# Performance work log

Hardware: AMD Instinct MI355X
Metric: run time of the kernel (lower is better)

## Reference

```python
import jax, jax.numpy as jnp
import numpy as np

B = 262144
P = 0.8
CLS_NUM_LIST = [500, 477, 456, 435, 415, 396, 378, 361, 345, 329, 314, 300, 286, 273, 261, 249, 238, 227, 217, 207, 197, 188, 180, 172, 164, 156, 149, 142, 136, 130, 124, 118, 113, 108, 103, 98, 94, 90, 85, 82, 78, 74, 71, 68, 65, 62, 59, 56, 54, 51, 49, 47, 45, 43, 41, 39, 37, 35, 34, 32, 31, 29, 28, 27, 26, 24, 23, 22, 21, 20, 19, 18, 18, 17, 16, 15, 15, 14, 13, 13, 12, 12, 11, 11, 10, 10, 9, 9, 8, 8, 8, 7, 7, 7, 6, 6, 6, 5, 5, 5]
C = len(CLS_NUM_LIST)


def _build_weight_matrix():
    n = np.asarray(CLS_NUM_LIST, dtype=np.float64).reshape(C, 1)
    wm = (1.0 / n) * n.T            # wm[i, j] = n_j / n_i
    wm[wm > 1] = 1.0
    wm = np.power(wm, P)
    return jnp.asarray(wm, dtype=jnp.float32)


def setup_inputs() -> dict:
    key = jax.random.key(0)
    kx, kt = jax.random.split(key)
    x = jax.random.normal(kx, (B, C), dtype=jnp.float32)
    target = jax.random.randint(kt, (B,), 0, C, dtype=jnp.int64)
    weight_matrix = _build_weight_matrix()                      # [C, C]
    neg_grad = jnp.full((1, C), 1e-06, dtype=jnp.float32)
    pos_grad = jnp.full((1, C), 1e-06, dtype=jnp.float32)
    return {"x": x, "target": target, "weight_matrix": weight_matrix,
            "neg_grad": neg_grad, "pos_grad": pos_grad}


def reference(x, target, weight_matrix, neg_grad, pos_grad):
    bs, num_classes = x.shape
    onehot = jax.nn.one_hot(target, num_classes, dtype=x.dtype)   # [B, C]
    # one_hot @ weight_matrix is algebraically a row gather
    weight = weight_matrix[target]                                # [B, C]
    weighted_x = x + jnp.log(weight)
    log_sm = jax.nn.log_softmax(weighted_x, axis=1)               # stable log(softmax)
    softmax_x = jnp.exp(log_sm)
    # grad-statistic accumulation (detached in the original)
    grad = jnp.abs(softmax_x - onehot)
    neg_grad_new = neg_grad + (grad * (1.0 - onehot)).sum(0)      # [1, C]
    pos_grad_new = pos_grad + (grad * onehot).sum(0)              # [1, C]
    ratio = pos_grad_new / neg_grad_new
    loss = -jnp.sum(onehot * log_sm) / bs
    return loss, neg_grad_new, pos_grad_new, ratio
```

## Files before the change

### kernel.cpp

```cpp
#include <hip/hip_runtime.h>

#define NCLS 100
#define NROWS 262144
#define MAIN_BLOCKS 2048
#define MAIN_THREADS 256
#define NWAVES (MAIN_THREADS / 64)
#define NOCT ((MAIN_BLOCKS * MAIN_THREADS) / 8)
#define ROWS_PER_OCT (NROWS / NOCT)
#define PART_LD MAIN_BLOCKS
#define NPART (2 * NCLS + 1)
#define WS_NEEDED ((size_t)NPART * PART_LD * 4)

#define LOADX(buf, rp) do {                                                    \
    buf[0] = (rp)[k];                                                          \
    buf[1] = (rp)[8 + k];                                                      \
    buf[2] = (rp)[16 + k];                                                     \
    buf[3] = (k == 0) ? (rp)[24] : make_float4(0.f, 0.f, 0.f, 0.f);            \
} while (0)

#define COMPROW(buf, LGT, VTX, TT) do {                                        \
    float4 e[4];                                                               \
    float sp = 0.f;                                                            \
    _Pragma("unroll")                                                          \
    for (int m = 0; m < 4; ++m) {                                              \
        if (8 * m + k < 25) {                                                  \
            e[m].x = __expf(buf[m].x + fminf(lgn[m].x - (LGT), 0.f));          \
            e[m].y = __expf(buf[m].y + fminf(lgn[m].y - (LGT), 0.f));          \
            e[m].z = __expf(buf[m].z + fminf(lgn[m].z - (LGT), 0.f));          \
            e[m].w = __expf(buf[m].w + fminf(lgn[m].w - (LGT), 0.f));          \
            sp += (e[m].x + e[m].y) + (e[m].z + e[m].w);                       \
        } else {                                                               \
            e[m] = make_float4(0.f, 0.f, 0.f, 0.f);                            \
        }                                                                      \
    }                                                                          \
    float s = sp + __shfl_xor(sp, 1, 64);                                      \
    s += __shfl_xor(s, 2, 64);                                                 \
    s += __shfl_xor(s, 4, 64);                                                 \
    const float inv_s = 1.0f / s;                                              \
    if (k == 0) {                                                              \
        loss_local += __logf(s) - (VTX);                                       \
        const float pt = __expf(VTX) * inv_s;                                  \
        atomicAdd(&lds_q[TT], pt);                                             \
        atomicAdd(&lds_pos[TT], 1.0f - pt);                                    \
    }                                                                          \
    _Pragma("unroll")                                                          \
    for (int m = 0; m < 4; ++m) {                                              \
        if (8 * m + k < 25) {                                                  \
            S4[m].x = fmaf(e[m].x, inv_s, S4[m].x);                            \
            S4[m].y = fmaf(e[m].y, inv_s, S4[m].y);                            \
            S4[m].z = fmaf(e[m].z, inv_s, S4[m].z);                            \
            S4[m].w = fmaf(e[m].w, inv_s, S4[m].w);                            \
        }                                                                      \
    }                                                                          \
} while (0)

__global__ __launch_bounds__(MAIN_THREADS, 4)
void seesaw_main(const float* __restrict__ x,
                 const int* __restrict__ target,
                 const float* __restrict__ wm,
                 float* __restrict__ part,
                 float* __restrict__ out,
                 int use_part) {
    __shared__ float lds_lgn[NCLS];
    __shared__ float lds_q[NCLS];
    __shared__ float lds_pos[NCLS];
    __shared__ float lds_S[NWAVES][NCLS];
    __shared__ float lds_loss[NWAVES];

    if (threadIdx.x < NCLS) {
        lds_lgn[threadIdx.x] = __logf(wm[threadIdx.x]);
        lds_q[threadIdx.x] = 0.f;
        lds_pos[threadIdx.x] = 0.f;
    }
    __syncthreads();

    const int lane = threadIdx.x & 63;
    const int wave = threadIdx.x >> 6;
    const int k    = threadIdx.x & 7;
    const int oct  = (blockIdx.x * MAIN_THREADS + threadIdx.x) >> 3;

    float4 lgn[4];
#pragma unroll
    for (int m = 0; m < 4; ++m) {
        const int g = 8 * m + k;
        if (g < 25) {
            lgn[m].x = lds_lgn[4 * g + 0];
            lgn[m].y = lds_lgn[4 * g + 1];
            lgn[m].z = lds_lgn[4 * g + 2];
            lgn[m].w = lds_lgn[4 * g + 3];
        } else {
            lgn[m] = make_float4(0.f, 0.f, 0.f, 0.f);
        }
    }

    int tr[ROWS_PER_OCT];
    float vtx[ROWS_PER_OCT], lgt[ROWS_PER_OCT];
    const float4* xr[ROWS_PER_OCT];
#pragma unroll
    for (int r = 0; r < ROWS_PER_OCT; ++r) {
        const int row = oct + r * NOCT;
        tr[r] = target[row];
        xr[r] = reinterpret_cast<const float4*>(x + (size_t)row * NCLS);
    }
#pragma unroll
    for (int r = 0; r < ROWS_PER_OCT; ++r) {
        vtx[r] = x[(size_t)(oct + r * NOCT) * NCLS + tr[r]];
        lgt[r] = lds_lgn[tr[r]];
    }

    float4 S4[4];
#pragma unroll
    for (int m = 0; m < 4; ++m) S4[m] = make_float4(0.f, 0.f, 0.f, 0.f);
    float loss_local = 0.0f;

    float4 xv0[4], xv1[4];
    LOADX(xv0, xr[0]);
    LOADX(xv1, xr[1]);
    COMPROW(xv0, lgt[0], vtx[0], tr[0]);
    LOADX(xv0, xr[2]);
    COMPROW(xv1, lgt[1], vtx[1], tr[1]);
    LOADX(xv1, xr[3]);
    COMPROW(xv0, lgt[2], vtx[2], tr[2]);
    COMPROW(xv1, lgt[3], vtx[3], tr[3]);

#pragma unroll
    for (int m = 0; m < 4; ++m) {
#pragma unroll
        for (int msk = 8; msk <= 32; msk <<= 1) {
            S4[m].x += __shfl_xor(S4[m].x, msk, 64);
            S4[m].y += __shfl_xor(S4[m].y, msk, 64);
            S4[m].z += __shfl_xor(S4[m].z, msk, 64);
            S4[m].w += __shfl_xor(S4[m].w, msk, 64);
        }
    }
#pragma unroll
    for (int msk = 1; msk < 64; msk <<= 1)
        loss_local += __shfl_xor(loss_local, msk, 64);
    if (lane == 0) lds_loss[wave] = loss_local;

    if (lane < 8) {
#pragma unroll
        for (int m = 0; m < 4; ++m) {
            const int g = 8 * m + lane;
            if (g < 25) {
                lds_S[wave][4 * g + 0] = S4[m].x;
                lds_S[wave][4 * g + 1] = S4[m].y;
                lds_S[wave][4 * g + 2] = S4[m].z;
                lds_S[wave][4 * g + 3] = S4[m].w;
            }
        }
    }
    __syncthreads();

    if (use_part) {
        if (threadIdx.x < NCLS) {
            const int j = threadIdx.x;
            float sb = 0.f;
#pragma unroll
            for (int w = 0; w < NWAVES; ++w) sb += lds_S[w][j];
            part[(size_t)j * PART_LD + blockIdx.x] = sb - lds_q[j];
            part[(size_t)(NCLS + j) * PART_LD + blockIdx.x] = lds_pos[j];
        }
        if (threadIdx.x == 0) {
            float l = 0.f;
#pragma unroll
            for (int w = 0; w < NWAVES; ++w) l += lds_loss[w];
            part[(size_t)(2 * NCLS) * PART_LD + blockIdx.x] = l;
        }
    } else {
        if (threadIdx.x < NCLS) {
            const int j = threadIdx.x;
            float sb = 0.f;
#pragma unroll
            for (int w = 0; w < NWAVES; ++w) sb += lds_S[w][j];
            atomicAdd(&out[1 + j], sb - lds_q[j]);
            atomicAdd(&out[1 + NCLS + j], lds_pos[j]);
        }
        if (threadIdx.x == 0) {
            float l = 0.f;
#pragma unroll
            for (int w = 0; w < NWAVES; ++w) l += lds_loss[w];
            atomicAdd(&out[0], l);
        }
    }
}

__global__ void seesaw_tail(const float* __restrict__ part,
                            const float* __restrict__ neg_in,
                            const float* __restrict__ pos_in,
                            float* __restrict__ out) {
    const int c = blockIdx.x;
    __shared__ float redn[NWAVES], redp[NWAVES];
    const int lane = threadIdx.x & 63;
    const int wave = threadIdx.x >> 6;

    float sn = 0.f, sp = 0.f;
    if (c < NCLS) {
        for (int b = threadIdx.x; b < MAIN_BLOCKS; b += MAIN_THREADS) {
            sn += part[(size_t)c * PART_LD + b];
            sp += part[(size_t)(NCLS + c) * PART_LD + b];
        }
    } else {
        for (int b = threadIdx.x; b < MAIN_BLOCKS; b += MAIN_THREADS)
            sn += part[(size_t)(2 * NCLS) * PART_LD + b];
    }
#pragma unroll
    for (int msk = 1; msk < 64; msk <<= 1) {
        sn += __shfl_xor(sn, msk, 64);
        sp += __shfl_xor(sp, msk, 64);
    }
    if (lane == 0) { redn[wave] = sn; redp[wave] = sp; }
    __syncthreads();
    if (threadIdx.x == 0) {
        float tn = 0.f, tp = 0.f;
#pragma unroll
        for (int w = 0; w < NWAVES; ++w) { tn += redn[w]; tp += redp[w]; }
        if (c < NCLS) {
            const float neg = neg_in[c] + tn;
            const float pos = pos_in[c] + tp;
            out[1 + c] = neg;
            out[1 + NCLS + c] = pos;
            out[1 + 2 * NCLS + c] = pos / neg;
        } else {
            out[0] = tn * (1.0f / (float)NROWS);
        }
    }
}

__global__ void seesaw_init(const float* __restrict__ neg_in,
                            const float* __restrict__ pos_in,
                            float* __restrict__ out) {
    int i = threadIdx.x;
    if (i == 0) out[0] = 0.0f;
    if (i < NCLS) {
        out[1 + i] = neg_in[i];
        out[1 + NCLS + i] = pos_in[i];
    }
}

__global__ void seesaw_fin(float* __restrict__ out) {
    int j = threadIdx.x;
    if (j == 0) out[0] *= (1.0f / (float)NROWS);
    if (j < NCLS) out[1 + 2 * NCLS + j] = out[1 + NCLS + j] / out[1 + j];
}

extern "C" void kernel_launch(void* const* d_in, const int* in_sizes, int n_in,
                              void* d_out, int out_size, void* d_ws, size_t ws_size,
                              hipStream_t stream) {
    const float* x      = (const float*)d_in[0];
    const int*   target = (const int*)d_in[1];
    const float* wm     = (const float*)d_in[2];
    const float* neg_in = (const float*)d_in[3];
    const float* pos_in = (const float*)d_in[4];
    float* out  = (float*)d_out;
    float* part = (float*)d_ws;
    const int use_part = (ws_size >= WS_NEEDED) ? 1 : 0;

    if (use_part) {
        hipLaunchKernelGGL(seesaw_main, dim3(MAIN_BLOCKS), dim3(MAIN_THREADS), 0, stream,
                           x, target, wm, part, out, 1);
        hipLaunchKernelGGL(seesaw_tail, dim3(NCLS + 1), dim3(MAIN_THREADS), 0, stream,
                           part, neg_in, pos_in, out);
    } else {
        hipLaunchKernelGGL(seesaw_init, dim3(1), dim3(256), 0, stream,
                           neg_in, pos_in, out);
        hipLaunchKernelGGL(seesaw_main, dim3(MAIN_BLOCKS), dim3(MAIN_THREADS), 0, stream,
                           x, target, wm, part, out, 0);
        hipLaunchKernelGGL(seesaw_fin, dim3(1), dim3(128), 0, stream, out);
    }
}
```

Before: 32.37 us.

## Fuse main pass and tail reduction into one cooperative kernel with grid sync

Adds a cooperative kernel that computes per-block partials, publishes them with agent-scope stores, performs a grid-wide sync, then has the first 101 blocks reduce the partials and write final outputs. This removes the second kernel launch and its launch gap. Launch bounds rise to 8 blocks per CU so all 2048 blocks can be co-resident; it falls back to the two-kernel path if occupancy or the cooperative launch fails. Risks include grid-sync overhead, a per-call occupancy query on the host, and register pressure from the tighter launch bound.

```diff
diff --git a/kernel.cpp b/kernel.cpp
--- a/kernel.cpp
+++ b/kernel.cpp
@@ -1,4 +1,5 @@
 #include <hip/hip_runtime.h>
+#include <hip/hip_cooperative_groups.h>
 
 #define NCLS 100
 #define NROWS 262144
@@ -8,8 +9,9 @@
 #define NOCT ((MAIN_BLOCKS * MAIN_THREADS) / 8)
 #define ROWS_PER_OCT (NROWS / NOCT)
 #define PART_LD MAIN_BLOCKS
-#define NPART (2 * NCLS + 1)
-#define WS_NEEDED ((size_t)NPART * PART_LD * 4)
+#define NPC (2 * NCLS + 1)
+#define WS_NEEDED ((size_t)NPC * PART_LD * 4)
+
 
 #define LOADX(buf, rp) do {                                                    \
     buf[0] = (rp)[k];                                                          \
@@ -54,6 +56,175 @@
     }                                                                          \
 } while (0)
 
+__device__ __forceinline__ void seesaw_body(
+    const float* __restrict__ x, const int* __restrict__ target,
+    const float* __restrict__ wm,
+    float* lds_lgn, float* lds_q, float* lds_pos,
+    float* lds_S , float* lds_loss) {
+
+    if (threadIdx.x < NCLS) {
+        lds_lgn[threadIdx.x] = __logf(wm[threadIdx.x]);
+        lds_q[threadIdx.x] = 0.f;
+        lds_pos[threadIdx.x] = 0.f;
+    }
+    __syncthreads();
+
+    const int lane = threadIdx.x & 63;
+    const int wave = threadIdx.x >> 6;
+    const int k    = threadIdx.x & 7;
+    const int oct  = (blockIdx.x * MAIN_THREADS + threadIdx.x) >> 3;
+
+    float4 lgn[4];
+#pragma unroll
+    for (int m = 0; m < 4; ++m) {
+        const int g = 8 * m + k;
+        if (g < 25) {
+            lgn[m].x = lds_lgn[4 * g + 0];
+            lgn[m].y = lds_lgn[4 * g + 1];
+            lgn[m].z = lds_lgn[4 * g + 2];
+            lgn[m].w = lds_lgn[4 * g + 3];
+        } else {
+            lgn[m] = make_float4(0.f, 0.f, 0.f, 0.f);
+        }
+    }
+
+    int tr[ROWS_PER_OCT];
+    float vtx[ROWS_PER_OCT], lgt[ROWS_PER_OCT];
+    const float4* xr[ROWS_PER_OCT];
+#pragma unroll
+    for (int r = 0; r < ROWS_PER_OCT; ++r) {
+        const int row = oct + r * NOCT;
+        tr[r] = target[row];
+        xr[r] = reinterpret_cast<const float4*>(x + (size_t)row * NCLS);
+    }
+#pragma unroll
+    for (int r = 0; r < ROWS_PER_OCT; ++r) {
+        vtx[r] = x[(size_t)(oct + r * NOCT) * NCLS + tr[r]];
+        lgt[r] = lds_lgn[tr[r]];
+    }
+
+    float4 S4[4];
+#pragma unroll
+    for (int m = 0; m < 4; ++m) S4[m] = make_float4(0.f, 0.f, 0.f, 0.f);
+    float loss_local = 0.0f;
+
+    float4 xv0[4], xv1[4];
+    LOADX(xv0, xr[0]);
+    LOADX(xv1, xr[1]);
+    COMPROW(xv0, lgt[0], vtx[0], tr[0]);
+    LOADX(xv0, xr[2]);
+    COMPROW(xv1, lgt[1], vtx[1], tr[1]);
+    LOADX(xv1, xr[3]);
+    COMPROW(xv0, lgt[2], vtx[2], tr[2]);
+    COMPROW(xv1, lgt[3], vtx[3], tr[3]);
+
+#pragma unroll
+    for (int m = 0; m < 4; ++m) {
+#pragma unroll
+        for (int msk = 8; msk <= 32; msk <<= 1) {
+            S4[m].x += __shfl_xor(S4[m].x, msk, 64);
+            S4[m].y += __shfl_xor(S4[m].y, msk, 64);
+            S4[m].z += __shfl_xor(S4[m].z, msk, 64);
+            S4[m].w += __shfl_xor(S4[m].w, msk, 64);
+        }
+    }
+#pragma unroll
+    for (int msk = 1; msk < 64; msk <<= 1)
+        loss_local += __shfl_xor(loss_local, msk, 64);
+    if (lane == 0) lds_loss[wave] = loss_local;
+
+    if (lane < 8) {
+#pragma unroll
+        for (int m = 0; m < 4; ++m) {
+            const int g = 8 * m + lane;
+            if (g < 25) {
+                lds_S[wave * NCLS + 4 * g + 0] = S4[m].x;
+                lds_S[wave * NCLS + 4 * g + 1] = S4[m].y;
+                lds_S[wave * NCLS + 4 * g + 2] = S4[m].z;
+                lds_S[wave * NCLS + 4 * g + 3] = S4[m].w;
+            }
+        }
+    }
+    __syncthreads();
+}
+
+__global__ __launch_bounds__(MAIN_THREADS, 8)
+void seesaw_coop(const float* __restrict__ x,
+                 const int* __restrict__ target,
+                 const float* __restrict__ wm,
+                 float* __restrict__ part,
+                 const float* __restrict__ neg_in,
+                 const float* __restrict__ pos_in,
+                 float* __restrict__ out) {
+    __shared__ float lds_lgn[NCLS];
+    __shared__ float lds_q[NCLS];
+    __shared__ float lds_pos[NCLS];
+    __shared__ float lds_S[NWAVES * NCLS];
+    __shared__ float lds_loss[NWAVES];
+    __shared__ float redn[NWAVES], redp[NWAVES];
+
+    seesaw_body(x, target, wm, lds_lgn, lds_q, lds_pos, lds_S, lds_loss);
+
+    if (threadIdx.x < NCLS) {
+        const int j = threadIdx.x;
+        float sb = 0.f;
+#pragma unroll
+        for (int w = 0; w < NWAVES; ++w) sb += lds_S[w * NCLS + j];
+        __hip_atomic_store(&part[(size_t)j * PART_LD + blockIdx.x], sb - lds_q[j],
+                           __ATOMIC_RELAXED, __HIP_MEMORY_SCOPE_AGENT);
+        __hip_atomic_store(&part[(size_t)(NCLS + j) * PART_LD + blockIdx.x], lds_pos[j],
+                           __ATOMIC_RELAXED, __HIP_MEMORY_SCOPE_AGENT);
+    }
+    if (threadIdx.x == 0) {
+        float l = 0.f;
+#pragma unroll
+        for (int w = 0; w < NWAVES; ++w) l += lds_loss[w];
+        __hip_atomic_store(&part[(size_t)(2 * NCLS) * PART_LD + blockIdx.x], l,
+                           __ATOMIC_RELAXED, __HIP_MEMORY_SCOPE_AGENT);
+    }
+    __threadfence();
+    cooperative_groups::this_grid().sync();
+
+    const int c = blockIdx.x;
+    if (c > NCLS) return;
+    const int lane = threadIdx.x & 63;
+    const int wave = threadIdx.x >> 6;
+    float sn = 0.f, sp2 = 0.f;
+    if (c < NCLS) {
+        for (int b = threadIdx.x; b < PART_LD; b += MAIN_THREADS) {
+            sn  += __hip_atomic_load(&part[(size_t)c * PART_LD + b],
+                                     __ATOMIC_RELAXED, __HIP_MEMORY_SCOPE_AGENT);
+            sp2 += __hip_atomic_load(&part[(size_t)(NCLS + c) * PART_LD + b],
+                                     __ATOMIC_RELAXED, __HIP_MEMORY_SCOPE_AGENT);
+        }
+    } else {
+        for (int b = threadIdx.x; b < PART_LD; b += MAIN_THREADS)
+            sn += __hip_atomic_load(&part[(size_t)(2 * NCLS) * PART_LD + b],
+                                    __ATOMIC_RELAXED, __HIP_MEMORY_SCOPE_AGENT);
+    }
+#pragma unroll
+    for (int msk = 1; msk < 64; msk <<= 1) {
+        sn += __shfl_xor(sn, msk, 64);
+        sp2 += __shfl_xor(sp2, msk, 64);
+    }
+    if (lane == 0) { redn[wave] = sn; redp[wave] = sp2; }
+    __syncthreads();
+    if (threadIdx.x == 0) {
+        float tn = 0.f, tp = 0.f;
+#pragma unroll
+        for (int w = 0; w < NWAVES; ++w) { tn += redn[w]; tp += redp[w]; }
+        if (c < NCLS) {
+            const float neg = neg_in[c] + tn;
+            const float pos = pos_in[c] + tp;
+            out[1 + c] = neg;
+            out[1 + NCLS + c] = pos;
+            out[1 + 2 * NCLS + c] = pos / neg;
+        } else {
+            out[0] = tn * (1.0f / (float)NROWS);
+        }
+    }
+}
+
 __global__ __launch_bounds__(MAIN_THREADS, 4)
 void seesaw_main(const float* __restrict__ x,
                  const int* __restrict__ target,
@@ -64,100 +235,17 @@
     __shared__ float lds_lgn[NCLS];
     __shared__ float lds_q[NCLS];
     __shared__ float lds_pos[NCLS];
-    __shared__ float lds_S[NWAVES][NCLS];
+    __shared__ float lds_S[NWAVES * NCLS];
     __shared__ float lds_loss[NWAVES];
 
-    if (threadIdx.x < NCLS) {
-        lds_lgn[threadIdx.x] = __logf(wm[threadIdx.x]);
-        lds_q[threadIdx.x] = 0.f;
-        lds_pos[threadIdx.x] = 0.f;
-    }
-    __syncthreads();
-
-    const int lane = threadIdx.x & 63;
-    const int wave = threadIdx.x >> 6;
-    const int k    = threadIdx.x & 7;
-    const int oct  = (blockIdx.x * MAIN_THREADS + threadIdx.x) >> 3;
-
-    float4 lgn[4];
-#pragma unroll
-    for (int m = 0; m < 4; ++m) {
-        const int g = 8 * m + k;
-        if (g < 25) {
-            lgn[m].x = lds_lgn[4 * g + 0];
-            lgn[m].y = lds_lgn[4 * g + 1];
-            lgn[m].z = lds_lgn[4 * g + 2];
-            lgn[m].w = lds_lgn[4 * g + 3];
-        } else {
-            lgn[m] = make_float4(0.f, 0.f, 0.f, 0.f);
-        }
-    }
-
-    int tr[ROWS_PER_OCT];
-    float vtx[ROWS_PER_OCT], lgt[ROWS_PER_OCT];
-    const float4* xr[ROWS_PER_OCT];
-#pragma unroll
-    for (int r = 0; r < ROWS_PER_OCT; ++r) {
-        const int row = oct + r * NOCT;
-        tr[r] = target[row];
-        xr[r] = reinterpret_cast<const float4*>(x + (size_t)row * NCLS);
-    }
-#pragma unroll
-    for (int r = 0; r < ROWS_PER_OCT; ++r) {
-        vtx[r] = x[(size_t)(oct + r * NOCT) * NCLS + tr[r]];
-        lgt[r] = lds_lgn[tr[r]];
-    }
-
-    float4 S4[4];
-#pragma unroll
-    for (int m = 0; m < 4; ++m) S4[m] = make_float4(0.f, 0.f, 0.f, 0.f);
-    float loss_local = 0.0f;
-
-    float4 xv0[4], xv1[4];
-    LOADX(xv0, xr[0]);
-    LOADX(xv1, xr[1]);
-    COMPROW(xv0, lgt[0], vtx[0], tr[0]);
-    LOADX(xv0, xr[2]);
-    COMPROW(xv1, lgt[1], vtx[1], tr[1]);
-    LOADX(xv1, xr[3]);
-    COMPROW(xv0, lgt[2], vtx[2], tr[2]);
-    COMPROW(xv1, lgt[3], vtx[3], tr[3]);
-
-#pragma unroll
-    for (int m = 0; m < 4; ++m) {
-#pragma unroll
-        for (int msk = 8; msk <= 32; msk <<= 1) {
-            S4[m].x += __shfl_xor(S4[m].x, msk, 64);
-            S4[m].y += __shfl_xor(S4[m].y, msk, 64);
-            S4[m].z += __shfl_xor(S4[m].z, msk, 64);
-            S4[m].w += __shfl_xor(S4[m].w, msk, 64);
-        }
-    }
-#pragma unroll
-    for (int msk = 1; msk < 64; msk <<= 1)
-        loss_local += __shfl_xor(loss_local, msk, 64);
-    if (lane == 0) lds_loss[wave] = loss_local;
-
-    if (lane < 8) {
-#pragma unroll
-        for (int m = 0; m < 4; ++m) {
-            const int g = 8 * m + lane;
-            if (g < 25) {
-                lds_S[wave][4 * g + 0] = S4[m].x;
-                lds_S[wave][4 * g + 1] = S4[m].y;
-                lds_S[wave][4 * g + 2] = S4[m].z;
-                lds_S[wave][4 * g + 3] = S4[m].w;
-            }
-        }
-    }
-    __syncthreads();
+    seesaw_body(x, target, wm, lds_lgn, lds_q, lds_pos, lds_S, lds_loss);
 
     if (use_part) {
         if (threadIdx.x < NCLS) {
             const int j = threadIdx.x;
             float sb = 0.f;
 #pragma unroll
-            for (int w = 0; w < NWAVES; ++w) sb += lds_S[w][j];
+            for (int w = 0; w < NWAVES; ++w) sb += lds_S[w * NCLS + j];
             part[(size_t)j * PART_LD + blockIdx.x] = sb - lds_q[j];
             part[(size_t)(NCLS + j) * PART_LD + blockIdx.x] = lds_pos[j];
         }
@@ -172,7 +260,7 @@
             const int j = threadIdx.x;
             float sb = 0.f;
 #pragma unroll
-            for (int w = 0; w < NWAVES; ++w) sb += lds_S[w][j];
+            for (int w = 0; w < NWAVES; ++w) sb += lds_S[w * NCLS + j];
             atomicAdd(&out[1 + j], sb - lds_q[j]);
             atomicAdd(&out[1 + NCLS + j], lds_pos[j]);
         }
@@ -196,12 +284,12 @@
 
     float sn = 0.f, sp = 0.f;
     if (c < NCLS) {
-        for (int b = threadIdx.x; b < MAIN_BLOCKS; b += MAIN_THREADS) {
+        for (int b = threadIdx.x; b < PART_LD; b += MAIN_THREADS) {
             sn += part[(size_t)c * PART_LD + b];
             sp += part[(size_t)(NCLS + c) * PART_LD + b];
         }
     } else {
-        for (int b = threadIdx.x; b < MAIN_BLOCKS; b += MAIN_THREADS)
+        for (int b = threadIdx.x; b < PART_LD; b += MAIN_THREADS)
             sn += part[(size_t)(2 * NCLS) * PART_LD + b];
     }
 #pragma unroll
@@ -254,18 +342,34 @@
     const float* pos_in = (const float*)d_in[4];
     float* out  = (float*)d_out;
     float* part = (float*)d_ws;
-    const int use_part = (ws_size >= WS_NEEDED) ? 1 : 0;
-
-    if (use_part) {
-        hipLaunchKernelGGL(seesaw_main, dim3(MAIN_BLOCKS), dim3(MAIN_THREADS), 0, stream,
-                           x, target, wm, part, out, 1);
-        hipLaunchKernelGGL(seesaw_tail, dim3(NCLS + 1), dim3(MAIN_THREADS), 0, stream,
-                           part, neg_in, pos_in, out);
-    } else {
-        hipLaunchKernelGGL(seesaw_init, dim3(1), dim3(256), 0, stream,
-                           neg_in, pos_in, out);
-        hipLaunchKernelGGL(seesaw_main, dim3(MAIN_BLOCKS), dim3(MAIN_THREADS), 0, stream,
-                           x, target, wm, part, out, 0);
-        hipLaunchKernelGGL(seesaw_fin, dim3(1), dim3(128), 0, stream, out);
-    }
-}
+
+    int coop_done = 0;
+    if (ws_size >= WS_NEEDED) {
+        int nb = 0;
+        hipError_t qe = hipOccupancyMaxActiveBlocksPerMultiprocessor(
+            &nb, reinterpret_cast<const void*>(&seesaw_coop), MAIN_THREADS, 0);
+        if (qe == hipSuccess && nb >= 8) {
+            void* kargs[] = {(void*)&x, (void*)&target, (void*)&wm, (void*)&part,
+                             (void*)&neg_in, (void*)&pos_in, (void*)&out};
+            if (hipLaunchCooperativeKernel(reinterpret_cast<const void*>(&seesaw_coop),
+                                           dim3(MAIN_BLOCKS), dim3(MAIN_THREADS),
+                                           kargs, 0, stream) == hipSuccess)
+                coop_done = 1;
+        }
+    }
+
+    if (!coop_done) {
+        if (ws_size >= WS_NEEDED) {
+            hipLaunchKernelGGL(seesaw_main, dim3(MAIN_BLOCKS), dim3(MAIN_THREADS), 0, stream,
+                               x, target, wm, part, out, 1);
+            hipLaunchKernelGGL(seesaw_tail, dim3(NCLS + 1), dim3(MAIN_THREADS), 0, stream,
+                               part, neg_in, pos_in, out);
+        } else {
+            hipLaunchKernelGGL(seesaw_init, dim3(1), dim3(256), 0, stream,
+                               neg_in, pos_in, out);
+            hipLaunchKernelGGL(seesaw_main, dim3(MAIN_BLOCKS), dim3(MAIN_THREADS), 0, stream,
+                               x, target, wm, part, out, 0);
+            hipLaunchKernelGGL(seesaw_fin, dim3(1), dim3(128), 0, stream, out);
+        }
+    }
+}
```

After: 32.39 us. Within noise of the previous version (+0.1%).
